# Optimization experiments

Measured on AMD Instinct MI355X. Metric: run time of the kernel, lower is better.

## Reference

```python
import jax, jax.numpy as jnp
import numpy as np

NUM_HEADS = 12
LN_EPS = 1e-5


def _depthwise_conv(x, w):
    # x: [N, H, W, C], w: [kh, kw, 1, C] (HWIO, feature_group_count=C)
    return jax.lax.conv_general_dilated(
        x, w, window_strides=(1, 1), padding=((1, 1), (1, 1)),
        dimension_numbers=('NHWC', 'HWIO', 'NHWC'),
        feature_group_count=x.shape[-1])


def _pool_norm(t, w, g, b, T, H, W):
    # t: [B, nh, L, hd] -> depthwise 2D conv over (H, W) per frame, then LayerNorm(hd)
    B, nh, L, hd = t.shape
    x = t.reshape(B * nh * T, H, W, hd)
    x = _depthwise_conv(x, w)
    x = x.reshape(B, nh, L, hd)
    mu = x.mean(-1, keepdims=True)
    var = x.var(-1, keepdims=True)
    return (x - mu) / jnp.sqrt(var + LN_EPS) * g + b


def _forward(x, qkv_w, out_w, out_b, q_pool_w, k_pool_w, v_pool_w,
             q_ln_g, q_ln_b, k_ln_g, k_ln_b, v_ln_g, v_ln_b,
             rel_pos_h, rel_pos_w, T, H, W):
    B, L, C = x.shape
    nh = NUM_HEADS
    hd = C // nh
    scale = hd ** -0.5
    S = H * W

    # QKV projection (no bias), split into heads: [B, nh, L, hd]
    qkv = (x @ qkv_w.T).reshape(B, L, 3, nh, hd).transpose(2, 0, 3, 1, 4)
    q, k, v = qkv[0], qkv[1], qkv[2]

    # Conv pooling (stride 1, same padding) + LayerNorm per head channel dim
    q = _pool_norm(q, q_pool_w, q_ln_g, q_ln_b, T, H, W)
    k = _pool_norm(k, k_pool_w, k_ln_g, k_ln_b, T, H, W)
    v = _pool_norm(v, v_pool_w, v_ln_g, v_ln_b, T, H, W)

    # Scaled dot-product scores: [B, nh, L, L]
    attn = jnp.einsum('bhqd,bhkd->bhqk', q * scale, k)

    # Decomposed relative position bias, added per temporal block (diagonal in T)
    dist_h = jnp.arange(H)[:, None] - jnp.arange(H)[None, :] + (H - 1)
    dist_w = jnp.arange(W)[:, None] - jnp.arange(W)[None, :] + (W - 1)
    Rh = rel_pos_h[dist_h]  # [H, H, hd]
    Rw = rel_pos_w[dist_w]  # [W, W, hd]
    q5 = q.reshape(B, nh, T, H, W, hd)
    rel_h = jnp.einsum('bntxyc,xkc->bntxyk', q5, Rh)  # [B, nh, T, H, W, H]
    rel_w = jnp.einsum('bntxyc,ykc->bntxyk', q5, Rw)  # [B, nh, T, H, W, W]
    bias = rel_h[..., :, None] + rel_w[..., None, :]   # [B, nh, T, H, W, H, W]
    bias = bias.reshape(B, nh, T, S, S).transpose(2, 0, 1, 3, 4)  # [T, B, nh, S, S]

    attn6 = attn.reshape(B, nh, T, S, T, S)
    idx = jnp.arange(T)
    attn6 = attn6.at[:, :, idx, :, idx, :].add(bias)  # only diagonal temporal blocks
    attn = jax.nn.softmax(attn6.reshape(B, nh, L, L), axis=-1)

    out = jnp.einsum('bhqk,bhkd->bhqd', attn, v)
    out = out + q  # residual_pool
    out = out.transpose(0, 2, 1, 3).reshape(B, L, C)
    return out @ out_w.T + out_b


def setup_inputs() -> dict:
    key = jax.random.key(0)
    ks = jax.random.split(key, 12)
    B, T, H, W = 2, 2, 28, 28
    C, nh = 768, NUM_HEADS
    hd = C // nh
    L = T * H * W
    s = 0.02
    return {
        'x': jax.random.normal(ks[0], (B, L, C), jnp.float32),
        'qkv_w': jax.random.normal(ks[1], (3 * C, C), jnp.float32) * s,
        'out_w': jax.random.normal(ks[2], (C, C), jnp.float32) * s,
        'out_b': jnp.zeros((C,), jnp.float32),
        'q_pool_w': jax.random.normal(ks[3], (3, 3, 1, hd), jnp.float32) * s,
        'k_pool_w': jax.random.normal(ks[4], (3, 3, 1, hd), jnp.float32) * s,
        'v_pool_w': jax.random.normal(ks[5], (3, 3, 1, hd), jnp.float32) * s,
        'q_ln_g': jnp.ones((hd,), jnp.float32),
        'q_ln_b': jnp.zeros((hd,), jnp.float32),
        'k_ln_g': jnp.ones((hd,), jnp.float32),
        'k_ln_b': jnp.zeros((hd,), jnp.float32),
        'v_ln_g': jnp.ones((hd,), jnp.float32),
        'v_ln_b': jnp.zeros((hd,), jnp.float32),
        'rel_pos_h': jax.random.normal(ks[6], (2 * H - 1, hd), jnp.float32) * s,
        'rel_pos_w': jax.random.normal(ks[7], (2 * W - 1, hd), jnp.float32) * s,
        'T': T, 'H': H, 'W': W,
    }


def reference(x, qkv_w, out_w, out_b, q_pool_w, k_pool_w, v_pool_w,
              q_ln_g, q_ln_b, k_ln_g, k_ln_b, v_ln_g, v_ln_b,
              rel_pos_h, rel_pos_w, T, H, W):
    return _forward(x, qkv_w, out_w, out_b, q_pool_w, k_pool_w, v_pool_w,
                    q_ln_g, q_ln_b, k_ln_g, k_ln_b, v_ln_g, v_ln_b,
                    rel_pos_h, rel_pos_w, T, H, W)
```

## Files before the change

kernel.cpp:

```cpp
#include <hip/hip_runtime.h>
#include <math.h>

#define B_ 2
#define T_ 2
#define H_ 28
#define W_ 28
#define S_ (H_*W_)
#define L_ (T_*S_)
#define C_ 768
#define NH_ 12
#define HD_ 64
#define LN_EPS 1e-5f
#define LOG2E 1.4426950408889634f
#define SCALE_K (0.125f * LOG2E)

typedef unsigned int uint_;
typedef unsigned int u32x2 __attribute__((ext_vector_type(2)));
typedef unsigned int u32x4 __attribute__((ext_vector_type(4)));
typedef __bf16 bf16x8 __attribute__((ext_vector_type(8)));
typedef float f32x4 __attribute__((ext_vector_type(4)));
typedef float f32x16 __attribute__((ext_vector_type(16)));

#define BC8(x) __builtin_bit_cast(bf16x8, (x))

__device__ __forceinline__ unsigned short f2bf(float f) {
  uint_ u = __builtin_bit_cast(uint_, f);
  u += 0x7FFFu + ((u >> 16) & 1u);
  return (unsigned short)(u >> 16);
}
__device__ __forceinline__ float bf2f(unsigned short h) {
  return __builtin_bit_cast(float, ((uint_)h) << 16);
}
__device__ __forceinline__ uint_ cvtpk(float a, float b) {
  uint_ r;
  asm("v_cvt_pk_bf16_f32 %0, %1, %2" : "=v"(r) : "v"(a), "v"(b));
  return r;
}
__device__ __forceinline__ void gload16(const void* g, void* l) {
  __builtin_amdgcn_global_load_lds(
      (const __attribute__((address_space(1))) unsigned int*)g,
      (__attribute__((address_space(3))) unsigned int*)l, 16, 0, 0);
}

__global__ __launch_bounds__(256) void cvt_all(
    const float* __restrict__ s0, int n0, unsigned short* __restrict__ d0,
    const float* __restrict__ s1, int n1, unsigned short* __restrict__ d1,
    const float* __restrict__ s2, int n2, unsigned short* __restrict__ d2) {
  int i = (blockIdx.x * 256 + threadIdx.x) * 8;
  const float* s; unsigned short* d;
  if (i < n0) { s = s0; d = d0; }
  else if (i < n0 + n1) { i -= n0; s = s1; d = d1; }
  else { i -= n0 + n1; if (i >= n2) return; s = s2; d = d2; }
  float4 a = *(const float4*)(s + i);
  float4 b = *(const float4*)(s + i + 4);
  u32x4 o;
  o.x = cvtpk(a.x, a.y); o.y = cvtpk(a.z, a.w);
  o.z = cvtpk(b.x, b.y); o.w = cvtpk(b.z, b.w);
  *(u32x4*)(d + i) = o;
}

__global__ __launch_bounds__(256) void cvt_rel(
    const float* __restrict__ rph, const float* __restrict__ rpw,
    unsigned short* __restrict__ Rhb, unsigned short* __restrict__ Rwb) {
  const int i = blockIdx.x * 256 + threadIdx.x;
  if (i >= 4096) return;
  const int j = i >> 6;
  const unsigned short vh = (j < 2*H_-1) ? f2bf(rph[i] * LOG2E) : 0;
  const unsigned short vw = (j < 2*W_-1) ? f2bf(rpw[i] * LOG2E) : 0;
  Rhb[i] = vh;
  Rwb[i] = vw;
}

__device__ __forceinline__ void gemm_core(
    const unsigned short* __restrict__ A, const unsigned short* __restrict__ Bm,
    int K, int m0, int n0, f32x4 (&acc)[4][4]) {
  __shared__ __align__(16) unsigned short As[128 * 32];
  __shared__ __align__(16) unsigned short Bs[128 * 32];
  const int tid = threadIdx.x;
  const int lane = tid & 63;
  const int wv = tid >> 6;
  const int wm = wv >> 1, wn = wv & 1;
  const int srow = tid >> 2, scol = (tid & 3) * 8;
  const int fr = lane & 15, fk = (lane >> 4) * 8;
  const unsigned short* ag = A + (size_t)(m0 + srow) * K + scol;
  const unsigned short* bg = Bm + (size_t)(n0 + srow) * K + scol;
  unsigned short* asd = As + tid * 8;
  unsigned short* bsd = Bs + tid * 8;
  const int arow = wm * 64 + fr;
  const int brow = wn * 64 + fr;
  for (int k0 = 0; k0 < K; k0 += 32) {
    __syncthreads();
    gload16(ag + k0, asd);
    gload16(ag + (size_t)64 * K + k0, asd + 2048);
    gload16(bg + k0, bsd);
    gload16(bg + (size_t)64 * K + k0, bsd + 2048);
    __syncthreads();
    bf16x8 af[4], bfr[4];
    #pragma unroll
    for (int m = 0; m < 4; ++m)
      af[m] = *(const bf16x8*)(As + (arow + m * 16) * 32 + fk);
    #pragma unroll
    for (int n = 0; n < 4; ++n)
      bfr[n] = *(const bf16x8*)(Bs + (brow + n * 16) * 32 + fk);
    #pragma unroll
    for (int m = 0; m < 4; ++m)
      #pragma unroll
      for (int n = 0; n < 4; ++n)
        acc[m][n] = __builtin_amdgcn_mfma_f32_16x16x32_bf16(af[m], bfr[n], acc[m][n], 0, 0, 0);
  }
}

__global__ __launch_bounds__(256) void qkv_gemm_mfma(
    const unsigned short* __restrict__ Xbf, const unsigned short* __restrict__ Wbf,
    float* __restrict__ q_raw, float* __restrict__ k_raw, float* __restrict__ v_raw) {
  f32x4 acc[4][4] = {};
  const int m0 = blockIdx.y * 128;
  const int n0 = blockIdx.x * 128;
  gemm_core(Xbf, Wbf, C_, m0, n0, acc);
  const int lane = threadIdx.x & 63;
  const int wv = threadIdx.x >> 6;
  const int wm = wv >> 1, wn = wv & 1;
  const int fr = lane & 15, fj = (lane >> 4) * 4;
  #pragma unroll
  for (int n = 0; n < 4; ++n) {
    const int gn = n0 + wn * 64 + n * 16 + fr;
    const int which = (gn >= 2 * C_) ? 2 : ((gn >= C_) ? 1 : 0);
    const int rem = gn - which * C_;
    const int h = rem >> 6, d = rem & 63;
    float* dst = (which == 0) ? q_raw : ((which == 1) ? k_raw : v_raw);
    #pragma unroll
    for (int m = 0; m < 4; ++m) {
      #pragma unroll
      for (int j = 0; j < 4; ++j) {
        const int gm = m0 + wm * 64 + m * 16 + fj + j;
        if (gm < B_ * L_) {
          const int b = (gm >= L_) ? 1 : 0;
          const int l = gm - b * L_;
          dst[(((size_t)b * NH_ + h) * L_ + l) * HD_ + d] = acc[m][n][j];
        }
      }
    }
  }
}

__global__ __launch_bounds__(256) void proj_gemm_mfma(
    const unsigned short* __restrict__ Abf, const unsigned short* __restrict__ Wobf,
    const float* __restrict__ bo, float* __restrict__ out) {
  f32x4 acc[4][4] = {};
  const int m0 = blockIdx.y * 128;
  const int n0 = blockIdx.x * 128;
  gemm_core(Abf, Wobf, C_, m0, n0, acc);
  const int lane = threadIdx.x & 63;
  const int wv = threadIdx.x >> 6;
  const int wm = wv >> 1, wn = wv & 1;
  const int fr = lane & 15, fj = (lane >> 4) * 4;
  #pragma unroll
  for (int n = 0; n < 4; ++n) {
    const int gn = n0 + wn * 64 + n * 16 + fr;
    const float bias = bo[gn];
    #pragma unroll
    for (int m = 0; m < 4; ++m) {
      #pragma unroll
      for (int j = 0; j < 4; ++j) {
        const int gm = m0 + wm * 64 + m * 16 + fj + j;
        if (gm < B_ * L_) out[(size_t)gm * C_ + gn] = acc[m][n][j] + bias;
      }
    }
  }
}

__global__ __launch_bounds__(256) void pool_ln_fused(
    const float* __restrict__ q_raw, const float* __restrict__ k_raw,
    const float* __restrict__ v_raw,
    const float* __restrict__ qw, const float* __restrict__ kw,
    const float* __restrict__ vw,
    const float* __restrict__ qg, const float* __restrict__ qb2,
    const float* __restrict__ kg, const float* __restrict__ kb2,
    const float* __restrict__ vg, const float* __restrict__ vb2,
    unsigned short* __restrict__ Qmain, unsigned short* __restrict__ Kpack,
    unsigned short* __restrict__ Vpack) {
  const int which = blockIdx.y;
  const float* in = (which == 0) ? q_raw : (which == 1) ? k_raw : v_raw;
  const float* w  = (which == 0) ? qw : (which == 1) ? kw : vw;
  const float* g  = (which == 0) ? qg : (which == 1) ? kg : vg;
  const float* bb = (which == 0) ? qb2 : (which == 1) ? kb2 : vb2;
  const float scale = (which == 1) ? SCALE_K : 1.f;

  const int quad = blockIdx.x * 4 + (threadIdx.x >> 6);
  const int d = threadIdx.x & 63;
  const int row0 = quad * 4;
  const int bh = row0 / L_;
  const int l0  = row0 % L_;
  const int t  = l0 / S_;
  const int sq = l0 % S_;
  const int x = sq / W_, y = sq % W_;
  const float* base = in + ((size_t)bh * L_ + t * S_) * HD_ + d;

  float acc0 = 0.f, acc1 = 0.f, acc2 = 0.f, acc3 = 0.f;
  #pragma unroll
  for (int dx = 0; dx < 3; ++dx) {
    const int xx = x + dx - 1;
    if (xx < 0 || xx >= H_) continue;
    const float* rb = base + (size_t)xx * W_ * HD_;
    const float w0 = w[(dx*3 + 0) * HD_ + d];
    const float w1 = w[(dx*3 + 1) * HD_ + d];
    const float w2 = w[(dx*3 + 2) * HD_ + d];
    const float cm1 = (y > 0)     ? rb[(y-1) * HD_] : 0.f;
    const float c0  = rb[(y+0) * HD_];
    const float c1  = rb[(y+1) * HD_];
    const float c2  = rb[(y+2) * HD_];
    const float c3  = rb[(y+3) * HD_];
    const float c4  = (y+4 < W_)  ? rb[(y+4) * HD_] : 0.f;
    acc0 += cm1*w0 + c0*w1 + c1*w2;
    acc1 += c0*w0  + c1*w1 + c2*w2;
    acc2 += c1*w0  + c2*w1 + c3*w2;
    acc3 += c2*w0  + c3*w1 + c4*w2;
  }
  float s0a = acc0, s0b = acc0*acc0, s1a = acc1, s1b = acc1*acc1;
  float s2a = acc2, s2b = acc2*acc2, s3a = acc3, s3b = acc3*acc3;
  #pragma unroll
  for (int off = 32; off; off >>= 1) {
    s0a += __shfl_xor(s0a, off); s0b += __shfl_xor(s0b, off);
    s1a += __shfl_xor(s1a, off); s1b += __shfl_xor(s1b, off);
    s2a += __shfl_xor(s2a, off); s2b += __shfl_xor(s2b, off);
    s3a += __shfl_xor(s3a, off); s3b += __shfl_xor(s3b, off);
  }
  const float gd = g[d], bd = bb[d];
  const float mu0 = s0a * (1.f/64.f), var0 = s0b * (1.f/64.f) - mu0*mu0;
  const float mu1 = s1a * (1.f/64.f), var1 = s1b * (1.f/64.f) - mu1*mu1;
  const float mu2 = s2a * (1.f/64.f), var2 = s2b * (1.f/64.f) - mu2*mu2;
  const float mu3 = s3a * (1.f/64.f), var3 = s3b * (1.f/64.f) - mu3*mu3;
  const float f0 = ((acc0 - mu0) * rsqrtf(var0 + LN_EPS) * gd + bd) * scale;
  const float f1 = ((acc1 - mu1) * rsqrtf(var1 + LN_EPS) * gd + bd) * scale;
  const float f2 = ((acc2 - mu2) * rsqrtf(var2 + LN_EPS) * gd + bd) * scale;
  const float f3 = ((acc3 - mu3) * rsqrtf(var3 + LN_EPS) * gd + bd) * scale;

  if (which == 1) {
    const unsigned short v0 = f2bf(f0), v1 = f2bf(f1);
    const unsigned short v2 = f2bf(f2), v3 = f2bf(f3);
    const int kt = l0 >> 5;
    const int c = d >> 4;
    const int lane2 = (((d >> 3) & 1) << 5) | (l0 & 31);
    unsigned short* kp = Kpack + ((((size_t)bh * 49 + kt) * 4 + c) * 64 + lane2) * 8 + (d & 7);
    kp[0] = v0; kp[8] = v1; kp[16] = v2; kp[24] = v3;
  } else if (which == 0) {
    Qmain[(size_t)(row0 + 0) * 64 + d] = f2bf(f0);
    Qmain[(size_t)(row0 + 1) * 64 + d] = f2bf(f1);
    Qmain[(size_t)(row0 + 2) * 64 + d] = f2bf(f2);
    Qmain[(size_t)(row0 + 3) * 64 + d] = f2bf(f3);
  } else {
    const int kt = l0 >> 5;
    const int c = ((d >> 5) << 1) | ((l0 >> 4) & 1);
    const int lane2 = (((l0 >> 3) & 1) << 5) | (d & 31);
    const int e = l0 & 7;
    u32x2 ov;
    ov.x = cvtpk(f0, f1);
    ov.y = cvtpk(f2, f3);
    *(u32x2*)(Vpack + ((((size_t)bh * 49 + kt) * 4 + c) * 64 + lane2) * 8 + e) = ov;
  }
}

__global__ __launch_bounds__(64) void relpos_mfma(
    const unsigned short* __restrict__ Qmain,
    const unsigned short* __restrict__ Rhb,
    const unsigned short* __restrict__ Rwb,
    unsigned short* __restrict__ QbiasPack) {
  __shared__ float P[16][128];
  const int qt16 = blockIdx.x;
  const int bt = blockIdx.y;
  const int bh = bt >> 1, t = bt & 1;
  const int lane = threadIdx.x;
  const int fr = lane & 15, fk = (lane >> 4) * 8;

  const size_t rowbase = (size_t)bh * L_ + t * S_ + qt16 * 16;
  const unsigned short* arow = Qmain + (rowbase + fr) * 64 + fk;
  const bf16x8 a0 = *(const bf16x8*)(arow);
  const bf16x8 a1 = *(const bf16x8*)(arow + 32);

  f32x4 acch[4] = {}, accw[4] = {};
  #pragma unroll
  for (int n = 0; n < 4; ++n) {
    const unsigned short* bh_ = Rhb + (n * 16 + fr) * 64 + fk;
    const unsigned short* bw_ = Rwb + (n * 16 + fr) * 64 + fk;
    acch[n] = __builtin_amdgcn_mfma_f32_16x16x32_bf16(a0, *(const bf16x8*)bh_, acch[n], 0, 0, 0);
    acch[n] = __builtin_amdgcn_mfma_f32_16x16x32_bf16(a1, *(const bf16x8*)(bh_ + 32), acch[n], 0, 0, 0);
    accw[n] = __builtin_amdgcn_mfma_f32_16x16x32_bf16(a0, *(const bf16x8*)bw_, accw[n], 0, 0, 0);
    accw[n] = __builtin_amdgcn_mfma_f32_16x16x32_bf16(a1, *(const bf16x8*)(bw_ + 32), accw[n], 0, 0, 0);
  }
  #pragma unroll
  for (int n = 0; n < 4; ++n)
    #pragma unroll
    for (int j = 0; j < 4; ++j) {
      P[(lane >> 4) * 4 + j][n * 16 + fr]      = acch[n][j];
      P[(lane >> 4) * 4 + j][64 + n * 16 + fr] = accw[n][j];
    }
  __syncthreads();

  if (lane < 56) {
    const int e0 = lane * 2;
    const int tb = e0 / 56;
    const int tw0 = e0 % 56;
    const int cb = e0 >> 4;
    const int hi2 = (e0 >> 3) & 1;
    const int ee = e0 & 7;
    #pragma unroll
    for (int r = 0; r < 16; ++r) {
      const int gl = t * S_ + qt16 * 16 + r;
      const int sq = qt16 * 16 + r;
      const int x = sq / W_, y = sq % W_;
      float v0 = 0.f, v1 = 0.f;
      if (tb == t) {
        if (tw0 < 28) {
          v0 = P[r][x - tw0 + 27];
          v1 = P[r][x - tw0 + 26];
        } else {
          const int k0 = tw0 - 28;
          v0 = P[r][64 + y - k0 + 27];
          v1 = P[r][64 + y - k0 + 26];
        }
      }
      const int lane2 = (hi2 << 5) | (gl & 31);
      unsigned short* dst = QbiasPack +
          ((((size_t)bh * 49 + (gl >> 5)) * 7 + cb) * 64 + lane2) * 8 + ee;
      *(uint_*)dst = cvtpk(v0, v1);
    }
  }
}

__device__ __forceinline__ void load_k(
    const unsigned short* kbase, int kt,
    u32x4& k0, u32x4& k1, u32x4& k2, u32x4& k3) {
  const unsigned short* kp = kbase + (size_t)kt * 2048;
  k0 = *(const u32x4*)(kp);
  k1 = *(const u32x4*)(kp + 512);
  k2 = *(const u32x4*)(kp + 1024);
  k3 = *(const u32x4*)(kp + 1536);
}

__device__ __forceinline__ void load_v(
    const unsigned short* vbase, int kt,
    u32x4& va, u32x4& vb, u32x4& vc, u32x4& vd) {
  const unsigned short* vp = vbase + (size_t)kt * 2048;
  va = *(const u32x4*)(vp);
  vb = *(const u32x4*)(vp + 512);
  vc = *(const u32x4*)(vp + 1024);
  vd = *(const u32x4*)(vp + 1536);
}

template<bool BIAS>
__device__ __forceinline__ f32x16 qk_tile(
    int kt, int lo, int hi, const u32x4 (&qf)[4],
    const unsigned short* __restrict__ qbias,
    u32x4 k0, u32x4 k1, u32x4 k2, u32x4 k3) {
  f32x16 s = {};
  s = __builtin_amdgcn_mfma_f32_32x32x16_bf16(BC8(k0), BC8(qf[0]), s, 0, 0, 0);
  s = __builtin_amdgcn_mfma_f32_32x32x16_bf16(BC8(k1), BC8(qf[1]), s, 0, 0, 0);
  s = __builtin_amdgcn_mfma_f32_32x32x16_bf16(BC8(k2), BC8(qf[2]), s, 0, 0, 0);
  s = __builtin_amdgcn_mfma_f32_32x32x16_bf16(BC8(k3), BC8(qf[3]), s, 0, 0, 0);
  if (BIAS) {
    const int kr = kt * 32 + lo;
    const int t = (kr >= S_) ? 1 : 0;
    const int sk = kr - t * S_;
    const int x = sk / W_, y = sk - x * W_;
    const int p1 = t*56 + x;
    const int p2 = t*56 + 28 + y;
    const uint_ v1 = 0x3F80u << ((p1 & 1) << 4);
    const uint_ v2 = 0x3F80u << ((p2 & 1) << 4);
    const int g1 = p1 >> 3, g2 = p2 >> 3;
    const int w1 = (p1 >> 1) & 3, w2 = (p2 >> 1) & 3;
    #pragma unroll
    for (int c = 0; c < 7; ++c) {
      const int gg = 2*c + hi;
      u32x4 oh;
      oh.x = ((g1 == gg && w1 == 0) ? v1 : 0u) | ((g2 == gg && w2 == 0) ? v2 : 0u);
      oh.y = ((g1 == gg && w1 == 1) ? v1 : 0u) | ((g2 == gg && w2 == 1) ? v2 : 0u);
      oh.z = ((g1 == gg && w1 == 2) ? v1 : 0u) | ((g2 == gg && w2 == 2) ? v2 : 0u);
      oh.w = ((g1 == gg && w1 == 3) ? v1 : 0u) | ((g2 == gg && w2 == 3) ? v2 : 0u);
      const u32x4 qb = *(const u32x4*)(qbias + c * 512);
      s = __builtin_amdgcn_mfma_f32_32x32x16_bf16(BC8(oh), BC8(qb), s, 0, 0, 0);
    }
  }
  return s;
}

__device__ __forceinline__ void sm_pv(
    const f32x16& s,
    u32x4 va, u32x4 vb, u32x4 vc, u32x4 vd,
    f32x16& acc0, f32x16& acc1, float& l_run) {
  uint_ pw0, pw1, pw2, pw3, pw4, pw5, pw6, pw7;
  {
    float a, b;
    a = exp2f(s[0]);  b = exp2f(s[1]);  l_run += a+b; pw0 = cvtpk(a,b);
    a = exp2f(s[2]);  b = exp2f(s[3]);  l_run += a+b; pw1 = cvtpk(a,b);
    a = exp2f(s[4]);  b = exp2f(s[5]);  l_run += a+b; pw2 = cvtpk(a,b);
    a = exp2f(s[6]);  b = exp2f(s[7]);  l_run += a+b; pw3 = cvtpk(a,b);
    a = exp2f(s[8]);  b = exp2f(s[9]);  l_run += a+b; pw4 = cvtpk(a,b);
    a = exp2f(s[10]); b = exp2f(s[11]); l_run += a+b; pw5 = cvtpk(a,b);
    a = exp2f(s[12]); b = exp2f(s[13]); l_run += a+b; pw6 = cvtpk(a,b);
    a = exp2f(s[14]); b = exp2f(s[15]); l_run += a+b; pw7 = cvtpk(a,b);
  }
  auto sA = __builtin_amdgcn_permlane32_swap(pw0, pw2, false, false);
  auto sB = __builtin_amdgcn_permlane32_swap(pw1, pw3, false, false);
  auto sC = __builtin_amdgcn_permlane32_swap(pw4, pw6, false, false);
  auto sD = __builtin_amdgcn_permlane32_swap(pw5, pw7, false, false);
  u32x4 pa0, pa1;
  pa0.x = sA[0]; pa0.y = sB[0]; pa0.z = sA[1]; pa0.w = sB[1];
  pa1.x = sC[0]; pa1.y = sD[0]; pa1.z = sC[1]; pa1.w = sD[1];

  acc0 = __builtin_amdgcn_mfma_f32_32x32x16_bf16(BC8(pa0), BC8(va), acc0, 0, 0, 0);
  acc0 = __builtin_amdgcn_mfma_f32_32x32x16_bf16(BC8(pa1), BC8(vb), acc0, 0, 0, 0);
  acc1 = __builtin_amdgcn_mfma_f32_32x32x16_bf16(BC8(pa0), BC8(vc), acc1, 0, 0, 0);
  acc1 = __builtin_amdgcn_mfma_f32_32x32x16_bf16(BC8(pa1), BC8(vd), acc1, 0, 0, 0);
}

__device__ __forceinline__ bool bias_needed(int kt, int qt) {
  const int kmin = (kt * 32 >= S_) ? 1 : 0;
  const int kmax = (kt * 32 + 31 >= S_) ? 1 : 0;
  const int qmin = (qt * 32 >= S_) ? 1 : 0;
  const int qmax = (qt * 32 + 31 >= S_) ? 1 : 0;
  return (kmin <= qmax) && (qmin <= kmax);
}

__global__ __launch_bounds__(256) void attn_mfma(
    const unsigned short* __restrict__ Qmain, const unsigned short* __restrict__ QbiasPack,
    const unsigned short* __restrict__ Kpack, const unsigned short* __restrict__ Vpack,
    unsigned short* __restrict__ Abf) {
  __shared__ float red_acc[3][32][64];
  __shared__ float red_l[4][32];

  const int id0 = blockIdx.x;
  const int swz = (id0 & 7) * 147 + (id0 >> 3);
  const int qt = swz % 49;
  const int bh = swz / 49;

  const int lane = threadIdx.x & 63;
  const int wv = threadIdx.x >> 6;
  const int lo = lane & 31, hi = lane >> 5;
  const int q0 = qt * 32;

  const unsigned short* qrow = Qmain + ((size_t)bh * L_ + q0 + lo) * 64 + hi * 8;
  u32x4 qf[4];
  #pragma unroll
  for (int c = 0; c < 4; ++c) qf[c] = *(const u32x4*)(qrow + c * 16);
  const unsigned short* qbias = QbiasPack + ((size_t)bh * 49 + qt) * 3584 + lane * 8;

  const unsigned short* kbase = Kpack + (size_t)bh * 49 * 2048 + lane * 8;
  const unsigned short* vbase = Vpack + (size_t)bh * 49 * 2048 + lane * 8;

  f32x16 acc0 = {}, acc1 = {};
  float l_run = 0.f;
  const int nt = (49 - wv + 3) >> 2;

  #define KT(j) (wv + 4 * (j))
  #define QK(j, K0, K1, K2, K3) \
    (bias_needed(KT(j), qt) \
      ? qk_tile<true>(KT(j), lo, hi, qf, qbias, K0, K1, K2, K3) \
      : qk_tile<false>(KT(j), lo, hi, qf, qbias, K0, K1, K2, K3))

  u32x4 kA0, kA1, kA2, kA3, kB0, kB1, kB2, kB3;
  u32x4 va, vb, vc, vd;

  load_k(kbase, KT(0), kA0, kA1, kA2, kA3);
  load_k(kbase, KT(1), kB0, kB1, kB2, kB3);
  f32x16 s_prev = QK(0, kA0, kA1, kA2, kA3);

  int j = 1;
  for (; j + 1 < nt; j += 2) {
    load_v(vbase, KT(j - 1), va, vb, vc, vd);
    f32x16 s_cur = QK(j, kB0, kB1, kB2, kB3);
    load_k(kbase, KT(j + 1), kA0, kA1, kA2, kA3);
    sm_pv(s_prev, va, vb, vc, vd, acc0, acc1, l_run);
    s_prev = s_cur;
    load_v(vbase, KT(j), va, vb, vc, vd);
    f32x16 s_cur2 = QK(j + 1, kA0, kA1, kA2, kA3);
    const int pf = (j + 2 < nt) ? j + 2 : nt - 1;
    load_k(kbase, KT(pf), kB0, kB1, kB2, kB3);
    sm_pv(s_prev, va, vb, vc, vd, acc0, acc1, l_run);
    s_prev = s_cur2;
  }
  if (j < nt) {
    load_v(vbase, KT(j - 1), va, vb, vc, vd);
    f32x16 s_cur = QK(j, kB0, kB1, kB2, kB3);
    sm_pv(s_prev, va, vb, vc, vd, acc0, acc1, l_run);
    s_prev = s_cur;
  }
  load_v(vbase, KT(nt - 1), va, vb, vc, vd);
  sm_pv(s_prev, va, vb, vc, vd, acc0, acc1, l_run);
  #undef QK
  #undef KT

  l_run += __shfl_xor(l_run, 32);

  if (hi == 0) red_l[wv][lo] = l_run;
  if (wv >= 1) {
    #pragma unroll
    for (int r = 0; r < 16; ++r) {
      const int row = (r & 3) + 8*(r >> 2) + 4*hi;
      red_acc[wv-1][row][lo]      = acc0[r];
      red_acc[wv-1][row][32 + lo] = acc1[r];
    }
  }
  __syncthreads();
  if (wv == 0) {
    const int b = bh / NH_, h = bh % NH_;
    #pragma unroll
    for (int r = 0; r < 16; ++r) {
      const int row = (r & 3) + 8*(r >> 2) + 4*hi;
      const float inv = 1.0f / (red_l[0][row] + red_l[1][row] +
                                red_l[2][row] + red_l[3][row]);
      const float o0 = (acc0[r] + red_acc[0][row][lo] +
                        red_acc[1][row][lo] + red_acc[2][row][lo]) * inv;
      const float o1 = (acc1[r] + red_acc[0][row][32+lo] +
                        red_acc[1][row][32+lo] + red_acc[2][row][32+lo]) * inv;
      const size_t qoff = ((size_t)bh * L_ + q0 + row) * 64 + lo;
      const size_t ooff = ((size_t)(b * L_ + q0 + row)) * C_ + h * 64 + lo;
      Abf[ooff]      = f2bf(o0 + bf2f(Qmain[qoff]));
      Abf[ooff + 32] = f2bf(o1 + bf2f(Qmain[qoff + 32]));
    }
  }
}

extern "C" void kernel_launch(void* const* d_in, const int* in_sizes, int n_in,
                              void* d_out, int out_size, void* d_ws, size_t ws_size,
                              hipStream_t stream) {
  const float* x         = (const float*)d_in[0];
  const float* qkv_w     = (const float*)d_in[1];
  const float* out_w     = (const float*)d_in[2];
  const float* out_b     = (const float*)d_in[3];
  const float* q_pool_w  = (const float*)d_in[4];
  const float* k_pool_w  = (const float*)d_in[5];
  const float* v_pool_w  = (const float*)d_in[6];
  const float* q_ln_g    = (const float*)d_in[7];
  const float* q_ln_b    = (const float*)d_in[8];
  const float* k_ln_g    = (const float*)d_in[9];
  const float* k_ln_b    = (const float*)d_in[10];
  const float* v_ln_g    = (const float*)d_in[11];
  const float* v_ln_b    = (const float*)d_in[12];
  const float* rel_pos_h = (const float*)d_in[13];
  const float* rel_pos_w = (const float*)d_in[14];

  float* R = (float*)d_ws;
  const size_t NQ = (size_t)B_ * NH_ * L_ * HD_;
  float* q_raw = R;
  unsigned short* Abf = (unsigned short*)R;
  float* k_raw = R + NQ;
  float* v_raw = R + 2*NQ;
  const size_t D_off = 3*NQ;
  unsigned short* Xbf   = (unsigned short*)(R + D_off);
  unsigned short* Qmain = (unsigned short*)(R + D_off);
  const size_t E_off = D_off + 1228800;
  unsigned short* Kpack = (unsigned short*)(R + E_off);
  const size_t F_off = E_off + 1204224;
  unsigned short* Wbf   = (unsigned short*)(R + F_off);
  unsigned short* Vpack = (unsigned short*)(R + F_off);
  const size_t G_off = F_off + 1204224;
  unsigned short* Wobf = (unsigned short*)(R + G_off);
  const size_t H_off = G_off + 294912;
  unsigned short* QbiasPack = (unsigned short*)(R + H_off);
  const size_t I_off = H_off + 2107392;
  unsigned short* Rhb = (unsigned short*)(R + I_off);
  unsigned short* Rwb = (unsigned short*)(R + I_off + 2048);

  cvt_all<<<2328, 256, 0, stream>>>(x, 3136*768, Xbf,
                                    qkv_w, 2304*768, Wbf,
                                    out_w, 768*768, Wobf);
  cvt_rel<<<16, 256, 0, stream>>>(rel_pos_h, rel_pos_w, Rhb, Rwb);
  qkv_gemm_mfma<<<dim3(18, 25), 256, 0, stream>>>(Xbf, Wbf, q_raw, k_raw, v_raw);
  pool_ln_fused<<<dim3(2352, 3), 256, 0, stream>>>(
      q_raw, k_raw, v_raw, q_pool_w, k_pool_w, v_pool_w,
      q_ln_g, q_ln_b, k_ln_g, k_ln_b, v_ln_g, v_ln_b, Qmain, Kpack, Vpack);
  relpos_mfma<<<dim3(49, 48), 64, 0, stream>>>(Qmain, Rhb, Rwb, QbiasPack);
  attn_mfma<<<1176, 256, 0, stream>>>(Qmain, QbiasPack, Kpack, Vpack, Abf);
  proj_gemm_mfma<<<dim3(6, 25), 256, 0, stream>>>(Abf, Wobf, out_b, (float*)d_out);
}
```

Measured before the change: 134.5 us.

## Store QKV intermediates in bf16 and stage per-tile query bias in LDS

Measured after the change: 132.8 us. No clear change (-1.3%).

```diff
diff --git a/kernel.cpp b/kernel.cpp
--- a/kernel.cpp
+++ b/kernel.cpp
@@ -112,7 +112,8 @@
 
 __global__ __launch_bounds__(256) void qkv_gemm_mfma(
     const unsigned short* __restrict__ Xbf, const unsigned short* __restrict__ Wbf,
-    float* __restrict__ q_raw, float* __restrict__ k_raw, float* __restrict__ v_raw) {
+    unsigned short* __restrict__ q_raw, unsigned short* __restrict__ k_raw,
+    unsigned short* __restrict__ v_raw) {
   f32x4 acc[4][4] = {};
   const int m0 = blockIdx.y * 128;
   const int n0 = blockIdx.x * 128;
@@ -127,7 +128,7 @@
     const int which = (gn >= 2 * C_) ? 2 : ((gn >= C_) ? 1 : 0);
     const int rem = gn - which * C_;
     const int h = rem >> 6, d = rem & 63;
-    float* dst = (which == 0) ? q_raw : ((which == 1) ? k_raw : v_raw);
+    unsigned short* dst = (which == 0) ? q_raw : ((which == 1) ? k_raw : v_raw);
     #pragma unroll
     for (int m = 0; m < 4; ++m) {
       #pragma unroll
@@ -136,7 +137,7 @@
         if (gm < B_ * L_) {
           const int b = (gm >= L_) ? 1 : 0;
           const int l = gm - b * L_;
-          dst[(((size_t)b * NH_ + h) * L_ + l) * HD_ + d] = acc[m][n][j];
+          dst[(((size_t)b * NH_ + h) * L_ + l) * HD_ + d] = f2bf(acc[m][n][j]);
         }
       }
     }
@@ -170,8 +171,8 @@
 }
 
 __global__ __launch_bounds__(256) void pool_ln_fused(
-    const float* __restrict__ q_raw, const float* __restrict__ k_raw,
-    const float* __restrict__ v_raw,
+    const unsigned short* __restrict__ q_raw, const unsigned short* __restrict__ k_raw,
+    const unsigned short* __restrict__ v_raw,
     const float* __restrict__ qw, const float* __restrict__ kw,
     const float* __restrict__ vw,
     const float* __restrict__ qg, const float* __restrict__ qb2,
@@ -180,7 +181,7 @@
     unsigned short* __restrict__ Qmain, unsigned short* __restrict__ Kpack,
     unsigned short* __restrict__ Vpack) {
   const int which = blockIdx.y;
-  const float* in = (which == 0) ? q_raw : (which == 1) ? k_raw : v_raw;
+  const unsigned short* in = (which == 0) ? q_raw : (which == 1) ? k_raw : v_raw;
   const float* w  = (which == 0) ? qw : (which == 1) ? kw : vw;
   const float* g  = (which == 0) ? qg : (which == 1) ? kg : vg;
   const float* bb = (which == 0) ? qb2 : (which == 1) ? kb2 : vb2;
@@ -194,23 +195,23 @@
   const int t  = l0 / S_;
   const int sq = l0 % S_;
   const int x = sq / W_, y = sq % W_;
-  const float* base = in + ((size_t)bh * L_ + t * S_) * HD_ + d;
+  const unsigned short* base = in + ((size_t)bh * L_ + t * S_) * HD_ + d;
 
   float acc0 = 0.f, acc1 = 0.f, acc2 = 0.f, acc3 = 0.f;
   #pragma unroll
   for (int dx = 0; dx < 3; ++dx) {
     const int xx = x + dx - 1;
     if (xx < 0 || xx >= H_) continue;
-    const float* rb = base + (size_t)xx * W_ * HD_;
+    const unsigned short* rb = base + (size_t)xx * W_ * HD_;
     const float w0 = w[(dx*3 + 0) * HD_ + d];
     const float w1 = w[(dx*3 + 1) * HD_ + d];
     const float w2 = w[(dx*3 + 2) * HD_ + d];
-    const float cm1 = (y > 0)     ? rb[(y-1) * HD_] : 0.f;
-    const float c0  = rb[(y+0) * HD_];
-    const float c1  = rb[(y+1) * HD_];
-    const float c2  = rb[(y+2) * HD_];
-    const float c3  = rb[(y+3) * HD_];
-    const float c4  = (y+4 < W_)  ? rb[(y+4) * HD_] : 0.f;
+    const float cm1 = (y > 0)     ? bf2f(rb[(y-1) * HD_]) : 0.f;
+    const float c0  = bf2f(rb[(y+0) * HD_]);
+    const float c1  = bf2f(rb[(y+1) * HD_]);
+    const float c2  = bf2f(rb[(y+2) * HD_]);
+    const float c3  = bf2f(rb[(y+3) * HD_]);
+    const float c4  = (y+4 < W_)  ? bf2f(rb[(y+4) * HD_]) : 0.f;
     acc0 += cm1*w0 + c0*w1 + c1*w2;
     acc1 += c0*w0  + c1*w1 + c2*w2;
     acc2 += c1*w0  + c2*w1 + c3*w2;
@@ -350,7 +351,7 @@
 template<bool BIAS>
 __device__ __forceinline__ f32x16 qk_tile(
     int kt, int lo, int hi, const u32x4 (&qf)[4],
-    const unsigned short* __restrict__ qbias,
+    const unsigned short* qbias_lds,
     u32x4 k0, u32x4 k1, u32x4 k2, u32x4 k3) {
   f32x16 s = {};
   s = __builtin_amdgcn_mfma_f32_32x32x16_bf16(BC8(k0), BC8(qf[0]), s, 0, 0, 0);
@@ -376,7 +377,7 @@
       oh.y = ((g1 == gg && w1 == 1) ? v1 : 0u) | ((g2 == gg && w2 == 1) ? v2 : 0u);
       oh.z = ((g1 == gg && w1 == 2) ? v1 : 0u) | ((g2 == gg && w2 == 2) ? v2 : 0u);
       oh.w = ((g1 == gg && w1 == 3) ? v1 : 0u) | ((g2 == gg && w2 == 3) ? v2 : 0u);
-      const u32x4 qb = *(const u32x4*)(qbias + c * 512);
+      const u32x4 qb = *(const u32x4*)(qbias_lds + c * 512);
       s = __builtin_amdgcn_mfma_f32_32x32x16_bf16(BC8(oh), BC8(qb), s, 0, 0, 0);
     }
   }
@@ -427,6 +428,7 @@
     unsigned short* __restrict__ Abf) {
   __shared__ float red_acc[3][32][64];
   __shared__ float red_l[4][32];
+  __shared__ __align__(16) unsigned short qb_lds[3584];
 
   const int id0 = blockIdx.x;
   const int swz = (id0 & 7) * 147 + (id0 >> 3);
@@ -438,11 +440,17 @@
   const int lo = lane & 31, hi = lane >> 5;
   const int q0 = qt * 32;
 
+  {
+    const unsigned short* src = QbiasPack + ((size_t)bh * 49 + qt) * 3584;
+    for (int i = wv; i < 7; i += 4)
+      gload16(src + i * 512 + lane * 8, qb_lds + i * 512);
+  }
+
   const unsigned short* qrow = Qmain + ((size_t)bh * L_ + q0 + lo) * 64 + hi * 8;
   u32x4 qf[4];
   #pragma unroll
   for (int c = 0; c < 4; ++c) qf[c] = *(const u32x4*)(qrow + c * 16);
-  const unsigned short* qbias = QbiasPack + ((size_t)bh * 49 + qt) * 3584 + lane * 8;
+  const unsigned short* qbias_lds = qb_lds + lane * 8;
 
   const unsigned short* kbase = Kpack + (size_t)bh * 49 * 2048 + lane * 8;
   const unsigned short* vbase = Vpack + (size_t)bh * 49 * 2048 + lane * 8;
@@ -451,11 +459,13 @@
   float l_run = 0.f;
   const int nt = (49 - wv + 3) >> 2;
 
+  __syncthreads();
+
   #define KT(j) (wv + 4 * (j))
   #define QK(j, K0, K1, K2, K3) \
     (bias_needed(KT(j), qt) \
-      ? qk_tile<true>(KT(j), lo, hi, qf, qbias, K0, K1, K2, K3) \
-      : qk_tile<false>(KT(j), lo, hi, qf, qbias, K0, K1, K2, K3))
+      ? qk_tile<true>(KT(j), lo, hi, qf, qbias_lds, K0, K1, K2, K3) \
+      : qk_tile<false>(KT(j), lo, hi, qf, qbias_lds, K0, K1, K2, K3))
 
   u32x4 kA0, kA1, kA2, kA3, kB0, kB1, kB2, kB3;
   u32x4 va, vb, vc, vd;
@@ -541,10 +551,10 @@
 
   float* R = (float*)d_ws;
   const size_t NQ = (size_t)B_ * NH_ * L_ * HD_;
-  float* q_raw = R;
+  unsigned short* q_raw = (unsigned short*)R;
   unsigned short* Abf = (unsigned short*)R;
-  float* k_raw = R + NQ;
-  float* v_raw = R + 2*NQ;
+  unsigned short* k_raw = (unsigned short*)(R + NQ);
+  unsigned short* v_raw = (unsigned short*)(R + 2*NQ);
   const size_t D_off = 3*NQ;
   unsigned short* Xbf   = (unsigned short*)(R + D_off);
   unsigned short* Qmain = (unsigned short*)(R + D_off);
```
